# Kernel optimization log

Measured on AMD Instinct MI355X. Metric: run time of the kernel, lower is better.

## Reference

```python
import jax, jax.numpy as jnp
import numpy as np

S = 4096       # sequence length
D = 1024       # d_model
H = 16         # heads
DK = 64        # d_k == d_v
VERY_SMOL_NUM = -1e9


def setup_inputs() -> dict:
    key = jax.random.key(0)
    ks = jax.random.split(key, 14)
    sd = 1.0 / np.sqrt(D)
    inp = {
        "V": jax.random.normal(ks[0], (S, D), jnp.float32),
        "K": jax.random.normal(ks[1], (S, D), jnp.float32),
        "Q": jax.random.normal(ks[2], (S, D), jnp.float32),
        # per-head projection weights, stored [in, out] (x @ W + b)
        "WQ": jax.random.normal(ks[3], (H, D, DK), jnp.float32) * sd,
        "bQ": jax.random.normal(ks[4], (H, DK), jnp.float32) * sd,
        "WK": jax.random.normal(ks[5], (H, D, DK), jnp.float32) * sd,
        "bK": jax.random.normal(ks[6], (H, DK), jnp.float32) * sd,
        "WV": jax.random.normal(ks[7], (H, D, DK), jnp.float32) * sd,
        "bV": jax.random.normal(ks[8], (H, DK), jnp.float32) * sd,
        "WO": jax.random.normal(ks[9], (D, D), jnp.float32) * sd,
        "bO": jax.random.normal(ks[10], (D,), jnp.float32) * sd,
    }
    return inp


def reference(V, K, Q, WQ, bQ, WK, bK, WV, bV, WO, bO):
    # per-head projections, vectorized over heads: [H, S, DK]
    q = jnp.einsum('sd,hdk->hsk', Q, WQ) + bQ[:, None, :]
    k = jnp.einsum('sd,hdk->hsk', K, WK) + bK[:, None, :]
    v = jnp.einsum('sd,hdk->hsk', V, WV) + bV[:, None, :]
    # full QK^T per head, scaled
    scores = jnp.einsum('hsk,htk->hst', q, k) / jnp.sqrt(jnp.float32(DK))
    # original bug faithfully preserved: with masked=True the causal additive
    # mask (triu(ones,1) * VERY_SMOL_NUM) is applied TWICE
    tri = jnp.triu(jnp.ones((S, S), jnp.float32), 1) * VERY_SMOL_NUM
    scores = scores + 2.0 * tri
    # torch Softmax(dim=1) on 2D [S,S] scores == softmax over keys (last dim)
    attn = jax.nn.softmax(scores, axis=-1)
    heads = jnp.einsum('hst,htv->hsv', attn, v)          # [H, S, DK]
    cat = heads.transpose(1, 0, 2).reshape(S, H * DK)    # concat over heads
    return cat @ WO + bO
```

## Files before the change

### kernel.cpp

```cpp
#include <hip/hip_runtime.h>

typedef unsigned short u16;
typedef unsigned int u32;
typedef __attribute__((ext_vector_type(8))) __bf16 bf16x8;
typedef __attribute__((ext_vector_type(4))) float f32x4;
typedef __attribute__((ext_vector_type(16))) float f32x16;

#define S_LEN 4096
#define D_MODEL 1024
#define NH 16
#define DHEAD 64

__device__ __forceinline__ u16 f2bf(float f){
  unsigned u = __float_as_uint(f);
  u += 0x7FFFu + ((u >> 16) & 1u);
  return (u16)(u >> 16);
}

__device__ __forceinline__ void gload_lds16(const void* g, void* l){
  __builtin_amdgcn_global_load_lds((const __attribute__((address_space(1))) void*)g,
                                   (__attribute__((address_space(3))) void*)l, 16, 0, 0);
}

__global__ __launch_bounds__(256) void cvt3_kernel(const float* __restrict__ q,
                                                   const float* __restrict__ k,
                                                   const float* __restrict__ v,
                                                   u16* __restrict__ oq,
                                                   u16* __restrict__ ok,
                                                   u16* __restrict__ ov){
  int z = blockIdx.y;
  const float* in = (z==0)? q : (z==1)? k : v;
  u16* out = (z==0)? oq : (z==1)? ok : ov;
  int i = blockIdx.x*256 + threadIdx.x;
  float4 w = reinterpret_cast<const float4*>(in)[i];
  ushort4 o;
  o.x = f2bf(w.x); o.y = f2bf(w.y); o.z = f2bf(w.z); o.w = f2bf(w.w);
  reinterpret_cast<ushort4*>(out)[i] = o;
}

__global__ __launch_bounds__(256) void tcvt_qkv_kernel(const float* __restrict__ wq,
                                                       const float* __restrict__ wk,
                                                       const float* __restrict__ wv,
                                                       u16* __restrict__ oq,
                                                       u16* __restrict__ ok,
                                                       u16* __restrict__ ov){
  int which = blockIdx.y;
  const float* in = (which==0)? wq : (which==1)? wk : wv;
  u16* out = (which==0)? oq : (which==1)? ok : ov;
  __shared__ float tile[64][67];
  int z = blockIdx.z;
  const float* inh = in + (size_t)z*1024*64;
  u16* outh = out + (size_t)z*1024*64;
  int tid = threadIdx.x;
  int r0 = blockIdx.x*64;
  #pragma unroll
  for (int c=0;c<4;c++){
    int cl = c*256 + tid;
    int row = cl >> 4, cc = (cl & 15) * 4;
    float4 v = *reinterpret_cast<const float4*>(inh + (size_t)(r0+row)*64 + cc);
    tile[row][cc+0]=v.x; tile[row][cc+1]=v.y; tile[row][cc+2]=v.z; tile[row][cc+3]=v.w;
  }
  __syncthreads();
  #pragma unroll
  for (int c=0;c<4;c++){
    int cl = c*256 + tid;
    int crow = cl >> 4, rc = (cl & 15) * 4;
    ushort4 o;
    o.x = f2bf(tile[rc+0][crow]);
    o.y = f2bf(tile[rc+1][crow]);
    o.z = f2bf(tile[rc+2][crow]);
    o.w = f2bf(tile[rc+3][crow]);
    *reinterpret_cast<ushort4*>(outh + (size_t)crow*1024 + r0 + rc) = o;
  }
}

__global__ __launch_bounds__(256) void tcvt_wo_kernel(const float* __restrict__ in,
                                                      u16* __restrict__ out){
  __shared__ float tile[64][67];
  int r0 = blockIdx.x*64, c0 = blockIdx.y*64;
  int tid = threadIdx.x;
  #pragma unroll
  for (int c=0;c<4;c++){
    int cl = c*256 + tid;
    int row = cl >> 4, cc = (cl & 15) * 4;
    float4 v = *reinterpret_cast<const float4*>(in + (size_t)(r0+row)*1024 + c0 + cc);
    tile[row][cc+0]=v.x; tile[row][cc+1]=v.y; tile[row][cc+2]=v.z; tile[row][cc+3]=v.w;
  }
  __syncthreads();
  #pragma unroll
  for (int c=0;c<4;c++){
    int cl = c*256 + tid;
    int crow = cl >> 4, rc = (cl & 15) * 4;
    ushort4 o;
    o.x = f2bf(tile[rc+0][crow]);
    o.y = f2bf(tile[rc+1][crow]);
    o.z = f2bf(tile[rc+2][crow]);
    o.w = f2bf(tile[rc+3][crow]);
    *reinterpret_cast<ushort4*>(out + (size_t)(c0+crow)*1024 + r0 + rc) = o;
  }
}

__global__ __launch_bounds__(512) void gemm_qkv_kernel(
    const u16* __restrict__ Qb, const u16* __restrict__ Kb, const u16* __restrict__ Vb,
    const u16* __restrict__ WtQ, const u16* __restrict__ WtK, const u16* __restrict__ WtV,
    const float* __restrict__ bQ, const float* __restrict__ bK, const float* __restrict__ bV,
    u16* __restrict__ qbuf, u16* __restrict__ kbuf, u16* __restrict__ vtb, float qscale){
  const int M = S_LEN, N = D_MODEL, K = D_MODEL;
  int z = blockIdx.z;
  const u16* A  = (z==0)? Qb  : (z==1)? Kb  : Vb;
  const u16* Bt = (z==0)? WtQ : (z==1)? WtK : WtV;
  const float* bias = (z==0)? bQ : (z==1)? bK : bV;
  float oscale = (z==0)? qscale : 1.0f;

  __shared__ __align__(16) unsigned char lsA[2][16384];
  __shared__ __align__(16) unsigned char lsB[2][16384];
  int tid = threadIdx.x;
  int bm = blockIdx.y * 128, bn = blockIdx.x * 128;
  int wave = tid >> 6, lane = tid & 63;
  int wm = (wave >> 1) * 32, wn = (wave & 1) * 64;
  int lrow = lane & 15, lgrp = lane >> 4;

  f32x4 acc[2][4] = {};

  auto STAGE = [&](int buf, int k0){
    #pragma unroll
    for (int c=0;c<4;c++){
      int id = c*512 + tid;
      int r = (id & 1023) >> 3;
      int kc = id & 7;
      int cs = (kc ^ (r & 7)) << 3;
      if (id < 1024)
        gload_lds16(A + (size_t)(bm+r)*K + k0 + cs, lsA[buf] + ((id & 1023) << 4));
      else
        gload_lds16(Bt + (size_t)(bn+r)*K + k0 + cs, lsB[buf] + ((id & 1023) << 4));
    }
  };

  STAGE(0, 0);
  int cur = 0;
  for (int k0 = 0; k0 < K; k0 += 64){
    __syncthreads();
    if (k0 + 64 < K) STAGE(cur^1, k0 + 64);
    #pragma unroll
    for (int ks=0;ks<2;ks++){
      bf16x8 af[2], bfr[4];
      #pragma unroll
      for (int i=0;i<2;i++){
        int ar = wm + i*16 + lrow;
        af[i] = *reinterpret_cast<const bf16x8*>(lsA[cur] + ((ar*128 + ks*64 + lgrp*16) ^ ((ar&7)<<4)));
      }
      #pragma unroll
      for (int j=0;j<4;j++){
        int br = wn + j*16 + lrow;
        bfr[j] = *reinterpret_cast<const bf16x8*>(lsB[cur] + ((br*128 + ks*64 + lgrp*16) ^ ((br&7)<<4)));
      }
      __builtin_amdgcn_s_setprio(1);
      #pragma unroll
      for (int i=0;i<2;i++)
        #pragma unroll
        for (int j=0;j<4;j++)
          acc[i][j] = __builtin_amdgcn_mfma_f32_16x16x32_bf16(af[i], bfr[j], acc[i][j], 0,0,0);
      __builtin_amdgcn_s_setprio(0);
    }
    cur ^= 1;
  }

  #pragma unroll
  for (int j=0;j<4;j++){
    int n = bn + wn + j*16 + lrow;
    float bv = bias[n];
    int hh = n >> 6, kk = n & 63;
    #pragma unroll
    for (int i=0;i<2;i++){
      int m0 = bm + wm + i*16 + lgrp*4;
      float v[4];
      #pragma unroll
      for (int r=0;r<4;r++) v[r] = (acc[i][j][r] + bv) * oscale;
      if (z < 2){
        u16* o = (z==0)? qbuf : kbuf;
        #pragma unroll
        for (int r=0;r<4;r++) o[((size_t)hh*M + m0 + r)*64 + kk] = f2bf(v[r]);
      } else {
        ushort4 p; p.x=f2bf(v[0]); p.y=f2bf(v[1]); p.z=f2bf(v[2]); p.w=f2bf(v[3]);
        *reinterpret_cast<ushort4*>(vtb + ((size_t)hh*64 + kk)*M + m0) = p;
      }
    }
  }
}

__global__ __launch_bounds__(512) void gemm_out_kernel(const u16* __restrict__ A,
                                                       const u16* __restrict__ Bt,
                                                       const float* __restrict__ bias,
                                                       float* __restrict__ dst,
                                                       int M, int N, int K){
  __shared__ __align__(16) unsigned char lsA[2][16384];
  __shared__ __align__(16) unsigned char lsB[2][16384];
  int tid = threadIdx.x;
  int bm = blockIdx.y * 128, bn = blockIdx.x * 128;
  int wave = tid >> 6, lane = tid & 63;
  int wm = (wave >> 1) * 32, wn = (wave & 1) * 64;
  int lrow = lane & 15, lgrp = lane >> 4;

  f32x4 acc[2][4] = {};

  auto STAGE = [&](int buf, int k0){
    #pragma unroll
    for (int c=0;c<4;c++){
      int id = c*512 + tid;
      int r = (id & 1023) >> 3;
      int kc = id & 7;
      int cs = (kc ^ (r & 7)) << 3;
      if (id < 1024)
        gload_lds16(A + (size_t)(bm+r)*K + k0 + cs, lsA[buf] + ((id & 1023) << 4));
      else
        gload_lds16(Bt + (size_t)(bn+r)*K + k0 + cs, lsB[buf] + ((id & 1023) << 4));
    }
  };

  STAGE(0, 0);
  int cur = 0;
  for (int k0 = 0; k0 < K; k0 += 64){
    __syncthreads();
    if (k0 + 64 < K) STAGE(cur^1, k0 + 64);
    #pragma unroll
    for (int ks=0;ks<2;ks++){
      bf16x8 af[2], bfr[4];
      #pragma unroll
      for (int i=0;i<2;i++){
        int ar = wm + i*16 + lrow;
        af[i] = *reinterpret_cast<const bf16x8*>(lsA[cur] + ((ar*128 + ks*64 + lgrp*16) ^ ((ar&7)<<4)));
      }
      #pragma unroll
      for (int j=0;j<4;j++){
        int br = wn + j*16 + lrow;
        bfr[j] = *reinterpret_cast<const bf16x8*>(lsB[cur] + ((br*128 + ks*64 + lgrp*16) ^ ((br&7)<<4)));
      }
      __builtin_amdgcn_s_setprio(1);
      #pragma unroll
      for (int i=0;i<2;i++)
        #pragma unroll
        for (int j=0;j<4;j++)
          acc[i][j] = __builtin_amdgcn_mfma_f32_16x16x32_bf16(af[i], bfr[j], acc[i][j], 0,0,0);
      __builtin_amdgcn_s_setprio(0);
    }
    cur ^= 1;
  }

  #pragma unroll
  for (int j=0;j<4;j++){
    int n = bn + wn + j*16 + lrow;
    float bv = bias[n];
    #pragma unroll
    for (int i=0;i<2;i++){
      int m0 = bm + wm + i*16 + lgrp*4;
      #pragma unroll
      for (int r=0;r<4;r++) dst[(size_t)(m0+r)*N + n] = acc[i][j][r] + bv;
    }
  }
}

__global__ __launch_bounds__(512, 2) void flash_attn_kernel(const u16* __restrict__ qb,
                                                            const u16* __restrict__ kb,
                                                            const u16* __restrict__ vtb,
                                                            u16* __restrict__ pO,
                                                            float2* __restrict__ pml){
  int b = blockIdx.x;
  int h = b & 15;
  int u = b >> 4;
  int qt = 15 - (u >> 2);
  int quarter = u & 3;
  int seg = qt + 1;
  int j0 = quarter * seg, j1 = j0 + seg;

  int tid = threadIdx.x, wave = tid >> 6, lane = tid & 63;
  int l31 = lane & 31, hi = lane >> 5;
  const u16* qh  = qb  + (size_t)h * S_LEN * 64;
  const u16* kh  = kb  + (size_t)h * S_LEN * 64;
  const u16* vth = vtb + (size_t)h * 64 * S_LEN;

  __shared__ __align__(16) unsigned char lsK[2][8192];
  __shared__ __align__(16) unsigned char lsV[2][8192];
  __shared__ __align__(16) unsigned char lsP[8][1024];
  unsigned char* Pw = lsP[wave];

  int qw = qt*256 + wave*32;

  bf16x8 qf[4];
  #pragma unroll
  for (int ks=0;ks<4;ks++)
    qf[ks] = *reinterpret_cast<const bf16x8*>(qh + (size_t)(qw + l31)*64 + ks*16 + hi*8);

  f32x16 oacc0 = {}, oacc1 = {};
  float m_run = -3e38f, l_run = 0.f;

  const int kvbase = hi*1024 + l31*16;
  const int prbase = hi*512  + l31*16;
  const int pwbase = l31*16  + hi*8;

  const int krow = tid & 63, kcol = (tid >> 6) << 3;

  auto STAGE = [&](int buf, int jj){
    int kv0 = jj*64;
    gload_lds16(kh + (size_t)(kv0 + krow)*64 + kcol, lsK[buf] + (tid << 4));
    gload_lds16(vth + (size_t)krow*S_LEN + kv0 + kcol, lsV[buf] + (tid << 4));
  };

  STAGE(0, j0);
  int cur = 0;
  for (int j = j0; j < j1; j++){
    __syncthreads();
    if (j + 1 < j1) STAGE(cur^1, j + 1);

    int kv0 = j*64;
    int rel0 = qw - kv0;
    int rel1 = rel0 - 32;
    if (rel0 >= 0){
      bool act1 = rel1 >= 0;
      const unsigned char* Kc = lsK[cur] + kvbase;
      const unsigned char* Vc = lsV[cur] + kvbase;

      f32x16 s0 = {}, s1 = {};
      __builtin_amdgcn_s_setprio(1);
      #pragma unroll
      for (int ks=0;ks<4;ks++){
        bf16x8 kf = *reinterpret_cast<const bf16x8*>(Kc + ks*2048);
        s0 = __builtin_amdgcn_mfma_f32_32x32x16_bf16(kf, qf[ks], s0, 0,0,0);
      }
      if (act1){
        #pragma unroll
        for (int ks=0;ks<4;ks++){
          bf16x8 kf = *reinterpret_cast<const bf16x8*>(Kc + ks*2048 + 512);
          s1 = __builtin_amdgcn_mfma_f32_32x32x16_bf16(kf, qf[ks], s1, 0,0,0);
        }
      }
      __builtin_amdgcn_s_setprio(0);

      if (rel0 == 0){
        #pragma unroll
        for (int reg=0;reg<16;reg++){
          int kvloc = (reg & 3) + 8*(reg >> 2) + 4*hi;
          if (kvloc > l31) s0[reg] = -3e38f;
        }
      }
      if (act1 && rel1 == 0){
        #pragma unroll
        for (int reg=0;reg<16;reg++){
          int kvloc = (reg & 3) + 8*(reg >> 2) + 4*hi;
          if (kvloc > l31) s1[reg] = -3e38f;
        }
      }

      float mx = -3e38f;
      #pragma unroll
      for (int reg=0;reg<16;reg++) mx = fmaxf(mx, s0[reg]);
      if (act1){
        #pragma unroll
        for (int reg=0;reg<16;reg++) mx = fmaxf(mx, s1[reg]);
      }
      mx = fmaxf(mx, __shfl_xor(mx, 32));

      if (!__all(mx <= m_run + 11.54f)){
        float mnew = fmaxf(m_run, mx);
        float al = __builtin_amdgcn_exp2f(m_run - mnew);
        m_run = mnew; l_run *= al;
        #pragma unroll
        for (int reg=0;reg<16;reg++){ oacc0[reg] *= al; oacc1[reg] *= al; }
      }

      float ps = 0.f;
      #pragma unroll
      for (int reg=0;reg<16;reg++){
        float e = __builtin_amdgcn_exp2f(s0[reg] - m_run);
        s0[reg] = e; ps += e;
      }
      if (act1){
        #pragma unroll
        for (int reg=0;reg<16;reg++){
          float e = __builtin_amdgcn_exp2f(s1[reg] - m_run);
          s1[reg] = e; ps += e;
        }
      }
      ps += __shfl_xor(ps, 32);
      l_run += ps;

      #pragma unroll
      for (int r2=0;r2<2;r2++){
        #pragma unroll
        for (int bq=0;bq<2;bq++){
          int bb = 2*r2 + bq;
          u32 w0p, w1p;
          asm("v_cvt_pk_bf16_f32 %0, %1, %2" : "=v"(w0p) : "v"(s0[4*bb+0]), "v"(s0[4*bb+1]));
          asm("v_cvt_pk_bf16_f32 %0, %1, %2" : "=v"(w1p) : "v"(s0[4*bb+2]), "v"(s0[4*bb+3]));
          uint2 pv; pv.x = w0p; pv.y = w1p;
          *reinterpret_cast<uint2*>(Pw + bq*512 + pwbase) = pv;
        }
        __builtin_amdgcn_s_setprio(1);
        bf16x8 pb = *reinterpret_cast<const bf16x8*>(Pw + prbase);
        bf16x8 vf0 = *reinterpret_cast<const bf16x8*>(Vc + r2*2048);
        bf16x8 vf1 = *reinterpret_cast<const bf16x8*>(Vc + r2*2048 + 512);
        oacc0 = __builtin_amdgcn_mfma_f32_32x32x16_bf16(vf0, pb, oacc0, 0,0,0);
        oacc1 = __builtin_amdgcn_mfma_f32_32x32x16_bf16(vf1, pb, oacc1, 0,0,0);
        __builtin_amdgcn_s_setprio(0);
      }

      if (act1){
        #pragma unroll
        for (int r2=0;r2<2;r2++){
          #pragma unroll
          for (int bq=0;bq<2;bq++){
            int bb = 2*r2 + bq;
            u32 w0p, w1p;
            asm("v_cvt_pk_bf16_f32 %0, %1, %2" : "=v"(w0p) : "v"(s1[4*bb+0]), "v"(s1[4*bb+1]));
            asm("v_cvt_pk_bf16_f32 %0, %1, %2" : "=v"(w1p) : "v"(s1[4*bb+2]), "v"(s1[4*bb+3]));
            uint2 pv; pv.x = w0p; pv.y = w1p;
            *reinterpret_cast<uint2*>(Pw + bq*512 + pwbase) = pv;
          }
          __builtin_amdgcn_s_setprio(1);
          bf16x8 pb = *reinterpret_cast<const bf16x8*>(Pw + prbase);
          bf16x8 vf0 = *reinterpret_cast<const bf16x8*>(Vc + (2+r2)*2048);
          bf16x8 vf1 = *reinterpret_cast<const bf16x8*>(Vc + (2+r2)*2048 + 512);
          oacc0 = __builtin_amdgcn_mfma_f32_32x32x16_bf16(vf0, pb, oacc0, 0,0,0);
          oacc1 = __builtin_amdgcn_mfma_f32_32x32x16_bf16(vf1, pb, oacc1, 0,0,0);
          __builtin_amdgcn_s_setprio(0);
        }
      }
    }
    cur ^= 1;
  }

  int q = qw + l31;
  if (hi == 0){
    float2 ml; ml.x = m_run; ml.y = l_run;
    pml[((size_t)quarter*NH + h)*S_LEN + q] = ml;
  }
  #pragma unroll
  for (int df=0;df<2;df++){
    #pragma unroll
    for (int q4=0;q4<4;q4++){
      float a0 = df ? oacc1[4*q4+0] : oacc0[4*q4+0];
      float a1 = df ? oacc1[4*q4+1] : oacc0[4*q4+1];
      float a2 = df ? oacc1[4*q4+2] : oacc0[4*q4+2];
      float a3 = df ? oacc1[4*q4+3] : oacc0[4*q4+3];
      u32 w0d, w1d;
      asm("v_cvt_pk_bf16_f32 %0, %1, %2" : "=v"(w0d) : "v"(a0), "v"(a1));
      asm("v_cvt_pk_bf16_f32 %0, %1, %2" : "=v"(w1d) : "v"(a2), "v"(a3));
      int dquad = df*8 + 2*q4 + hi;
      uint2 pv; pv.x = w0d; pv.y = w1d;
      *reinterpret_cast<uint2*>(pO + (((size_t)(quarter*NH + h)*16 + dquad)*S_LEN + q)*4) = pv;
    }
  }
}

__global__ __launch_bounds__(256) void combine_kernel(const u16* __restrict__ pO,
                                                      const float2* __restrict__ pml,
                                                      u16* __restrict__ catb){
  int tid = threadIdx.x;
  int dq = tid & 15, qo = tid >> 4;
  int h = blockIdx.y;
  int q = blockIdx.x*16 + qo;
  float2 ml[4];
  #pragma unroll
  for (int i=0;i<4;i++) ml[i] = pml[((size_t)i*NH + h)*S_LEN + q];
  float m = fmaxf(fmaxf(ml[0].x, ml[1].x), fmaxf(ml[2].x, ml[3].x));
  float w[4], denom = 0.f;
  #pragma unroll
  for (int i=0;i<4;i++){ w[i] = __builtin_amdgcn_exp2f(ml[i].x - m); denom += w[i]*ml[i].y; }
  float inv = 1.0f / denom;
  float x0=0.f, x1=0.f, x2=0.f, x3=0.f;
  #pragma unroll
  for (int i=0;i<4;i++){
    ushort4 a = reinterpret_cast<const ushort4*>(pO)[((size_t)i*NH*16 + (size_t)h*16 + dq)*S_LEN + q];
    x0 += __uint_as_float((u32)a.x << 16) * w[i];
    x1 += __uint_as_float((u32)a.y << 16) * w[i];
    x2 += __uint_as_float((u32)a.z << 16) * w[i];
    x3 += __uint_as_float((u32)a.w << 16) * w[i];
  }
  ushort4 o;
  o.x = f2bf(x0*inv); o.y = f2bf(x1*inv); o.z = f2bf(x2*inv); o.w = f2bf(x3*inv);
  *reinterpret_cast<ushort4*>(catb + (size_t)q*D_MODEL + h*64 + dq*4) = o;
}

extern "C" void kernel_launch(void* const* d_in, const int* in_sizes, int n_in,
                              void* d_out, int out_size, void* d_ws, size_t ws_size,
                              hipStream_t stream){
  (void)in_sizes; (void)n_in; (void)out_size; (void)ws_size;
  const float* V  = (const float*)d_in[0];
  const float* Km = (const float*)d_in[1];
  const float* Q  = (const float*)d_in[2];
  const float* WQ = (const float*)d_in[3];
  const float* bQ = (const float*)d_in[4];
  const float* WK = (const float*)d_in[5];
  const float* bK = (const float*)d_in[6];
  const float* WV = (const float*)d_in[7];
  const float* bV = (const float*)d_in[8];
  const float* WO = (const float*)d_in[9];
  const float* bO = (const float*)d_in[10];
  float* out = (float*)d_out;

  char* ws = (char*)d_ws;
  const size_t SZ_SD = (size_t)S_LEN * D_MODEL * 2;
  const size_t SZ_W  = (size_t)D_MODEL * D_MODEL * 2;
  u16* Qb   = (u16*)(ws);
  u16* Kb   = (u16*)(ws + SZ_SD);
  u16* Vb   = (u16*)(ws + 2*SZ_SD);
  u16* WtQ  = (u16*)(ws + 3*SZ_SD);
  u16* WtK  = (u16*)(ws + 3*SZ_SD + SZ_W);
  u16* WtV  = (u16*)(ws + 3*SZ_SD + 2*SZ_W);
  u16* WtO  = (u16*)(ws + 3*SZ_SD + 3*SZ_W);
  u16* qbuf = (u16*)(ws + 3*SZ_SD + 4*SZ_W);
  u16* kbuf = (u16*)(ws + 4*SZ_SD + 4*SZ_W);
  u16* vtb  = (u16*)(ws + 5*SZ_SD + 4*SZ_W);
  u16* catb = (u16*)(ws + 6*SZ_SD + 4*SZ_W);
  u16* pO   = (u16*)(ws + 7*SZ_SD + 4*SZ_W);
  float2* pml = (float2*)(ws + 11*SZ_SD + 4*SZ_W);

  const float QSCALE = 0.18033688011112042f;

  cvt3_kernel<<<dim3(4096,3),256,0,stream>>>(Q, Km, V, Qb, Kb, Vb);
  tcvt_qkv_kernel<<<dim3(16,3,16),256,0,stream>>>(WQ, WK, WV, WtQ, WtK, WtV);
  tcvt_wo_kernel<<<dim3(16,16),256,0,stream>>>(WO, WtO);
  gemm_qkv_kernel<<<dim3(8,32,3),512,0,stream>>>(Qb, Kb, Vb, WtQ, WtK, WtV,
                                                 bQ, bK, bV, qbuf, kbuf, vtb, QSCALE);
  flash_attn_kernel<<<dim3(1024),512,0,stream>>>(qbuf, kbuf, vtb, pO, pml);
  combine_kernel<<<dim3(256,16),256,0,stream>>>(pO, pml, catb);
  gemm_out_kernel<<<dim3(8,32),512,0,stream>>>(catb, WtO, bO, out, S_LEN, D_MODEL, D_MODEL);
}
```

Baseline: 156.4 us.

## Split causal KV range into fixed 8-tile chunks instead of quarters

Replaces the four-way split of each query tile's causal KV range with fixed chunks of up to 8 KV tiles, giving 72 chunks per head and 1152 blocks in total. Each block now covers a roughly uniform amount of work, which is meant to even out load across CUs and reduce the tail. The combine kernel now merges a variable number of partials per query tile using an online max/rescale loop. The partial O and m/l buffers are re-laid out per block, and the combine step does more work for late query tiles.

```diff
diff --git a/kernel.cpp b/kernel.cpp
--- a/kernel.cpp
+++ b/kernel.cpp
@@ -10,6 +10,7 @@
 #define D_MODEL 1024
 #define NH 16
 #define DHEAD 64
+#define NCHUNK 72
 
 __device__ __forceinline__ u16 f2bf(float f){
   unsigned u = __float_as_uint(f);
@@ -266,11 +267,13 @@
                                                             float2* __restrict__ pml){
   int b = blockIdx.x;
   int h = b & 15;
-  int u = b >> 4;
-  int qt = 15 - (u >> 2);
-  int quarter = u & 3;
-  int seg = qt + 1;
-  int j0 = quarter * seg, j1 = j0 + seg;
+  int g = b >> 4;
+  int qt = 0;
+  #pragma unroll
+  for (int k=1;k<16;k++) if ((((k+1)*(k+1))>>2) <= g) qt = k;
+  int c = g - (((qt+1)*(qt+1))>>2);
+  int j0 = 8*c;
+  int j1 = min(8*c + 8, 4*qt + 4);
 
   int tid = threadIdx.x, wave = tid >> 6, lane = tid & 63;
   int l31 = lane & 31, hi = lane >> 5;
@@ -296,7 +299,6 @@
   const int kvbase = hi*1024 + l31*16;
   const int prbase = hi*512  + l31*16;
   const int pwbase = l31*16  + hi*8;
-
   const int krow = tid & 63, kcol = (tid >> 6) << 3;
 
   auto STAGE = [&](int buf, int jj){
@@ -428,10 +430,10 @@
     cur ^= 1;
   }
 
-  int q = qw + l31;
+  int row = wave*32 + l31;
   if (hi == 0){
     float2 ml; ml.x = m_run; ml.y = l_run;
-    pml[((size_t)quarter*NH + h)*S_LEN + q] = ml;
+    pml[(size_t)b*256 + row] = ml;
   }
   #pragma unroll
   for (int df=0;df<2;df++){
@@ -446,7 +448,7 @@
       asm("v_cvt_pk_bf16_f32 %0, %1, %2" : "=v"(w1d) : "v"(a2), "v"(a3));
       int dquad = df*8 + 2*q4 + hi;
       uint2 pv; pv.x = w0d; pv.y = w1d;
-      *reinterpret_cast<uint2*>(pO + (((size_t)(quarter*NH + h)*16 + dquad)*S_LEN + q)*4) = pv;
+      *reinterpret_cast<uint2*>(pO + (((size_t)b*16 + dquad)*256 + row)*4) = pv;
     }
   }
 }
@@ -458,23 +460,27 @@
   int dq = tid & 15, qo = tid >> 4;
   int h = blockIdx.y;
   int q = blockIdx.x*16 + qo;
-  float2 ml[4];
-  #pragma unroll
-  for (int i=0;i<4;i++) ml[i] = pml[((size_t)i*NH + h)*S_LEN + q];
-  float m = fmaxf(fmaxf(ml[0].x, ml[1].x), fmaxf(ml[2].x, ml[3].x));
-  float w[4], denom = 0.f;
-  #pragma unroll
-  for (int i=0;i<4;i++){ w[i] = __builtin_amdgcn_exp2f(ml[i].x - m); denom += w[i]*ml[i].y; }
-  float inv = 1.0f / denom;
+  int qt = q >> 8;
+  int row = q & 255;
+  int nch = (qt + 2) >> 1;
+  int gbase = ((qt+1)*(qt+1)) >> 2;
+  float m = -3e38f, l = 0.f;
   float x0=0.f, x1=0.f, x2=0.f, x3=0.f;
-  #pragma unroll
-  for (int i=0;i<4;i++){
-    ushort4 a = reinterpret_cast<const ushort4*>(pO)[((size_t)i*NH*16 + (size_t)h*16 + dq)*S_LEN + q];
-    x0 += __uint_as_float((u32)a.x << 16) * w[i];
-    x1 += __uint_as_float((u32)a.y << 16) * w[i];
-    x2 += __uint_as_float((u32)a.z << 16) * w[i];
-    x3 += __uint_as_float((u32)a.w << 16) * w[i];
-  }
+  for (int cc=0; cc<nch; cc++){
+    int bb = (gbase + cc)*16 + h;
+    float2 mlr = pml[(size_t)bb*256 + row];
+    ushort4 a = *reinterpret_cast<const ushort4*>(pO + (((size_t)bb*16 + dq)*256 + row)*4);
+    float mn = fmaxf(m, mlr.x);
+    float sa = __builtin_amdgcn_exp2f(m - mn);
+    float sb = __builtin_amdgcn_exp2f(mlr.x - mn);
+    l  = l*sa  + mlr.y*sb;
+    x0 = x0*sa + __uint_as_float((u32)a.x << 16)*sb;
+    x1 = x1*sa + __uint_as_float((u32)a.y << 16)*sb;
+    x2 = x2*sa + __uint_as_float((u32)a.z << 16)*sb;
+    x3 = x3*sa + __uint_as_float((u32)a.w << 16)*sb;
+    m = mn;
+  }
+  float inv = 1.0f / l;
   ushort4 o;
   o.x = f2bf(x0*inv); o.y = f2bf(x1*inv); o.z = f2bf(x2*inv); o.w = f2bf(x3*inv);
   *reinterpret_cast<ushort4*>(catb + (size_t)q*D_MODEL + h*64 + dq*4) = o;
@@ -512,7 +518,7 @@
   u16* vtb  = (u16*)(ws + 5*SZ_SD + 4*SZ_W);
   u16* catb = (u16*)(ws + 6*SZ_SD + 4*SZ_W);
   u16* pO   = (u16*)(ws + 7*SZ_SD + 4*SZ_W);
-  float2* pml = (float2*)(ws + 11*SZ_SD + 4*SZ_W);
+  float2* pml = (float2*)(ws + 7*SZ_SD + 4*SZ_W + (size_t)1152*16*256*4*2);
 
   const float QSCALE = 0.18033688011112042f;
 
@@ -521,7 +527,7 @@
   tcvt_wo_kernel<<<dim3(16,16),256,0,stream>>>(WO, WtO);
   gemm_qkv_kernel<<<dim3(8,32,3),512,0,stream>>>(Qb, Kb, Vb, WtQ, WtK, WtV,
                                                  bQ, bK, bV, qbuf, kbuf, vtb, QSCALE);
-  flash_attn_kernel<<<dim3(1024),512,0,stream>>>(qbuf, kbuf, vtb, pO, pml);
+  flash_attn_kernel<<<dim3(16*NCHUNK),512,0,stream>>>(qbuf, kbuf, vtb, pO, pml);
   combine_kernel<<<dim3(256,16),256,0,stream>>>(pO, pml, catb);
   gemm_out_kernel<<<dim3(8,32),512,0,stream>>>(catb, WtO, bO, out, S_LEN, D_MODEL, D_MODEL);
 }
```

Result: slower. 163.6 us (+4.6%).
